# Optimization experiments

Measured on AMD Instinct MI355X. Metric: run time of the kernel, lower is better.

Reference implementation:

```python
import jax, jax.numpy as jnp
import numpy as np

N, E, D, H, L = 50000, 800000, 64, 1, 4
R_DIMS = [64, 32, 16, 16]
LN_EPS = 1e-6  # flax LayerNorm default


def _ln(x, s, b):
    m = jnp.mean(x, axis=-1, keepdims=True)
    v = jnp.mean(jnp.square(x - m), axis=-1, keepdims=True)
    return (x - m) / jnp.sqrt(v + LN_EPS) * s + b


def _jat_layer(x, edges, senders, receivers, mask, Wq, Wk, Wa, ln_s, ln_b, readout):
    # x: (N, H, D) node features
    n = x.shape[0]
    q = jnp.einsum('nab,abcd->ncd', x, Wq)   # (N, H, D) query projection
    k = jnp.einsum('nab,abcd->ncd', x, Wk)   # (N, H, D) key projection
    sq = q[senders]                           # (E, H, D) gather by sender
    rk = k[receivers]                         # (E, H, D) gather by receiver
    feat = jax.nn.swish(sq + rk)
    # per-head edge distance powers, as in the original code
    ep = jnp.reshape(jnp.stack([jnp.power(edges, i + 1) for i in range(H)], axis=0), (-1, H, 1))
    feat = jnp.concatenate([feat, ep], axis=-1)       # (E, H, D+1)
    logits = jnp.einsum('eab,abcd->ecd', feat, Wa)    # (E, H, 1)
    logits = logits + jnp.reshape(jnp.where(mask, 0.0, -jnp.inf), (-1, 1, 1))
    # segment softmax over receiver segments (stable)
    maxs = jax.ops.segment_max(logits, receivers, n)
    w = jnp.exp(logits - maxs[receivers])
    w = w / jax.ops.segment_sum(w, receivers, n)[receivers]
    new = jax.ops.segment_sum(sq * w, receivers, n)   # (N, H, D)
    new = jax.nn.swish(new) + x  # skip_proj is identity (same n_head, dim)
    if not readout:
        new = _ln(new, ln_s, ln_b)
    return new


def setup_inputs() -> dict:
    key = jax.random.key(0)
    ks = jax.random.split(key, 32)
    inp = {
        'nodes': jax.random.normal(ks[0], (N, D), jnp.float32),
        'edges': jax.random.uniform(ks[1], (E, 1), jnp.float32, 0.1, 5.0),
        'senders': jax.random.randint(ks[2], (E,), 0, N, jnp.int32),
        'receivers': jax.random.randint(ks[3], (E,), 0, N, jnp.int32),
        'mask': jnp.ones((E,), bool),
        'Wq': jax.random.normal(ks[4], (L, H, D, H, D), jnp.float32) / np.sqrt(D).astype(np.float32),
        'Wk': jax.random.normal(ks[5], (L, H, D, H, D), jnp.float32) / np.sqrt(D).astype(np.float32),
        'Wa': jax.random.normal(ks[6], (L, H, D + 1, H, 1), jnp.float32) / np.sqrt(D + 1).astype(np.float32),
        'ln_scale': jnp.ones((L - 1, D), jnp.float32),
        'ln_bias': jnp.zeros((L - 1, D), jnp.float32),
    }
    dims = [H * D] + R_DIMS
    for i in range(4):
        inp[f'Wr{i}'] = jax.random.normal(ks[7 + i], (dims[i], dims[i + 1]), jnp.float32) / np.sqrt(dims[i]).astype(np.float32)
        inp[f'rs{i}'] = jnp.ones((dims[i + 1],), jnp.float32)
        inp[f'rb{i}'] = jnp.zeros((dims[i + 1],), jnp.float32)
    inp['Wr4'] = jax.random.normal(ks[11], (R_DIMS[-1], 1), jnp.float32) / np.sqrt(R_DIMS[-1]).astype(np.float32)
    return inp


def reference(nodes, edges, senders, receivers, mask, Wq, Wk, Wa, ln_scale, ln_bias,
              Wr0, Wr1, Wr2, Wr3, Wr4, rs0, rs1, rs2, rs3, rb0, rb1, rb2, rb3):
    x = nodes[:, None, :]  # (N, 1, D): stack to head axis (first layer)
    for l in range(L):
        readout = (l == L - 1)
        ln_s = ln_scale[l] if not readout else None
        ln_b = ln_bias[l] if not readout else None
        x = _jat_layer(x, edges, senders, receivers, mask, Wq[l], Wk[l], Wa[l], ln_s, ln_b, readout)
    # pyramidal readout head [64:32:16:16:1]
    h = jnp.reshape(x, (x.shape[0], -1))
    for Wd, s, b in zip((Wr0, Wr1, Wr2, Wr3), (rs0, rs1, rs2, rs3), (rb0, rb1, rb2, rb3)):
        h = jax.nn.swish(_ln(h @ Wd, s, b))
    return jax.nn.swish(h @ Wr4)  # (N, 1) atomic contributions
```

## Files before the change

### kernel.cpp

```cpp
#include <hip/hip_runtime.h>

#define NN 50000
#define EE 800000

typedef unsigned short ushort_t;
typedef unsigned int uint_t;

__device__ __forceinline__ float rcpf(float x) {
    float r; asm("v_rcp_f32 %0, %1" : "=v"(r) : "v"(x)); return r;
}
__device__ __forceinline__ float swishf(float v) {
    return v * rcpf(1.f + __expf(-v));
}
__device__ __forceinline__ ushort_t f2bf(float f) {
    uint_t u = __float_as_uint(f);
    return (ushort_t)((u + 0x7fffu + ((u >> 16) & 1u)) >> 16);
}
__device__ __forceinline__ float bf2f(ushort_t h) {
    return __uint_as_float(((uint_t)h) << 16);
}
__device__ __forceinline__ float rlane(float v, int i) {
    return __int_as_float(__builtin_amdgcn_readlane(__float_as_int(v), i));
}

__global__ void __launch_bounds__(256, 2) qk_kernel(
    const float* __restrict__ x, const float* __restrict__ Wq, const float* __restrict__ Wk,
    ushort_t* __restrict__ qbf, float* __restrict__ k)
{
    const int lane = threadIdx.x & 63;
    const int wave = (blockIdx.x * 256 + threadIdx.x) >> 6;
    const int nw = gridDim.x * 4;
    float wq[64], wk[64];
#pragma unroll
    for (int i = 0; i < 64; ++i) { wq[i] = Wq[i * 64 + lane]; wk[i] = Wk[i * 64 + lane]; }
    for (int row = wave; row < NN; row += nw) {
        const float h = x[(size_t)row * 64 + lane];
        float aq0 = 0.f, aq1 = 0.f, ak0 = 0.f, ak1 = 0.f;
#pragma unroll
        for (int i = 0; i < 64; i += 2) {
            const float h0 = rlane(h, i), h1 = rlane(h, i + 1);
            aq0 = fmaf(h0, wq[i], aq0);     ak0 = fmaf(h0, wk[i], ak0);
            aq1 = fmaf(h1, wq[i + 1], aq1); ak1 = fmaf(h1, wk[i + 1], ak1);
        }
        qbf[(size_t)row * 64 + lane] = f2bf(aq0 + aq1);
        k[(size_t)row * 64 + lane] = ak0 + ak1;
    }
}

__global__ void __launch_bounds__(256) hist_kernel(
    const int* __restrict__ receivers, int* __restrict__ counts)
{
    int e = blockIdx.x * 256 + threadIdx.x;
    int stride = gridDim.x * 256;
    for (; e < EE; e += stride) atomicAdd(counts + receivers[e], 1);
}

__global__ void __launch_bounds__(256) scanA_kernel(
    const int* __restrict__ counts, int* __restrict__ bsum)
{
    const int idx = blockIdx.x * 256 + threadIdx.x;
    const int lane = threadIdx.x & 63;
    const int wid = threadIdx.x >> 6;
    int s = (idx < NN) ? counts[idx] : 0;
#pragma unroll
    for (int m = 32; m; m >>= 1) s += __shfl_xor(s, m);
    __shared__ int ws[4];
    if (lane == 0) ws[wid] = s;
    __syncthreads();
    if (threadIdx.x == 0) bsum[blockIdx.x] = ws[0] + ws[1] + ws[2] + ws[3];
}

__global__ void __launch_bounds__(256) scanB_kernel(
    const int* __restrict__ bsum, int* __restrict__ boff,
    int* __restrict__ offsets, int nb)
{
    __shared__ int ts[256];
    const int t = threadIdx.x;
    const int v = (t < nb) ? bsum[t] : 0;
    ts[t] = v;
    __syncthreads();
#pragma unroll
    for (int d = 1; d < 256; d <<= 1) {
        const int o = (t >= d) ? ts[t - d] : 0;
        __syncthreads();
        ts[t] += o;
        __syncthreads();
    }
    if (t < nb) boff[t] = ts[t] - v;
    if (t == 0) offsets[NN] = EE;
}

__global__ void __launch_bounds__(256) scanC_kernel(
    const int* __restrict__ counts, const int* __restrict__ boff,
    int* __restrict__ offsets)
{
    const int idx = blockIdx.x * 256 + threadIdx.x;
    const int lane = threadIdx.x & 63;
    const int wid = threadIdx.x >> 6;
    const int v = (idx < NN) ? counts[idx] : 0;
    int incl = v;
#pragma unroll
    for (int d = 1; d < 64; d <<= 1) {
        const int o = __shfl_up(incl, d);
        if (lane >= d) incl += o;
    }
    __shared__ int ws[4];
    if (lane == 63) ws[wid] = incl;
    __syncthreads();
    int wpre = 0;
#pragma unroll
    for (int w = 0; w < 4; ++w) wpre += (w < wid) ? ws[w] : 0;
    if (idx < NN) offsets[idx] = boff[blockIdx.x] + wpre + incl - v;
}

__global__ void __launch_bounds__(256) scatter_kernel(
    const int* __restrict__ receivers, const int* __restrict__ senders,
    const float* __restrict__ edges, const int* __restrict__ offsets,
    int* __restrict__ ctr, int2* __restrict__ sesort)
{
    int e = blockIdx.x * 256 + threadIdx.x;
    int stride = gridDim.x * 256;
    for (; e < EE; e += stride) {
        int r = receivers[e];
        int pos = atomicAdd(ctr + r, 1);
        sesort[offsets[r] + pos] = make_int2(senders[e], __float_as_int(edges[e]));
    }
}

__global__ void __launch_bounds__(256) attn_kernel(
    const ushort_t* __restrict__ qbf, const float* __restrict__ k,
    const int2* __restrict__ sesort, const int* __restrict__ offsets,
    const float* __restrict__ Wa,
    float* __restrict__ x, const float* __restrict__ ln_s,
    const float* __restrict__ ln_b, int do_ln)
{
    __shared__ ushort_t sQ[4][8][64];
    __shared__ float sWb[4][8];
    const int lane = threadIdx.x & 63;
    const int winb = threadIdx.x >> 6;
    const int wave = (blockIdx.x * 256 + threadIdx.x) >> 6;
    const int nw = gridDim.x * 4;
    const int c = lane & 7;
    const int e = lane >> 3;
    const int ofs = c * 8;
    float wac[8];
#pragma unroll
    for (int j = 0; j < 8; ++j) wac[j] = Wa[ofs + j];
    const float wa64 = Wa[64];
    const float lnsv = ln_s[lane], lnbv = ln_b[lane];

    for (int r = wave; r < NN; r += nw) {
        float kc[8];
        {
            const float4 k0 = *(const float4*)(k + (size_t)r * 64 + ofs);
            const float4 k1 = *(const float4*)(k + (size_t)r * 64 + ofs + 4);
            kc[0] = k0.x; kc[1] = k0.y; kc[2] = k0.z; kc[3] = k0.w;
            kc[4] = k1.x; kc[5] = k1.y; kc[6] = k1.z; kc[7] = k1.w;
        }
        const float xv = x[(size_t)r * 64 + lane];
        const int beg = offsets[r], end = offsets[r + 1];
        float m = -3.0e38f, denp = 0.f, acc = 0.f;

        bool valid = (beg + e) < end;
        int2 sev = make_int2(0, 0);
        if (valid) sev = sesort[beg + e];
        uint4 qraw = *(const uint4*)(qbf + (size_t)sev.x * 64 + ofs);
        float ea = __int_as_float(sev.y);

        int i0 = beg;
        while (i0 < end) {
            const int ni0 = i0 + 8;
            bool nvalid = false; float nea = 0.f;
            uint4 nqraw = qraw;
            if (ni0 < end) {
                nvalid = (ni0 + e) < end;
                int2 nsev = make_int2(0, 0);
                if (nvalid) nsev = sesort[ni0 + e];
                nqraw = *(const uint4*)(qbf + (size_t)nsev.x * 64 + ofs);
                nea = __int_as_float(nsev.y);
            }
            float qv[8];
            qv[0] = __uint_as_float(qraw.x << 16);
            qv[1] = __uint_as_float(qraw.x & 0xFFFF0000u);
            qv[2] = __uint_as_float(qraw.y << 16);
            qv[3] = __uint_as_float(qraw.y & 0xFFFF0000u);
            qv[4] = __uint_as_float(qraw.z << 16);
            qv[5] = __uint_as_float(qraw.z & 0xFFFF0000u);
            qv[6] = __uint_as_float(qraw.w << 16);
            qv[7] = __uint_as_float(qraw.w & 0xFFFF0000u);
            float p = 0.f;
#pragma unroll
            for (int j = 0; j < 8; ++j) p = fmaf(swishf(qv[j] + kc[j]), wac[j], p);
            p += __shfl_xor(p, 1);
            p += __shfl_xor(p, 2);
            p += __shfl_xor(p, 4);
            const float logit = valid ? fmaf(ea, wa64, p) : -3.0e38f;
            float cm = logit;
            cm = fmaxf(cm, __shfl_xor(cm, 8));
            cm = fmaxf(cm, __shfl_xor(cm, 16));
            cm = fmaxf(cm, __shfl_xor(cm, 32));
            if (cm > m) {
                const float sc = __expf(m - cm);
                denp *= sc; acc *= sc; m = cm;
            }
            const float w = valid ? __expf(logit - m) : 0.f;
            denp += w;
            *(uint4*)(&sQ[winb][e][ofs]) = qraw;
            if (c == 0) sWb[winb][e] = w;
            __builtin_amdgcn_wave_barrier();
#pragma unroll
            for (int j = 0; j < 8; ++j)
                acc = fmaf(sWb[winb][j], bf2f(sQ[winb][j][lane]), acc);
            __builtin_amdgcn_wave_barrier();
            qraw = nqraw; ea = nea; valid = nvalid; i0 = ni0;
        }

        float den = denp;
#pragma unroll
        for (int msk = 32; msk; msk >>= 1) den += __shfl_xor(den, msk);
        den *= 0.125f;
        float v = den > 0.f ? acc * rcpf(den) : 0.f;
        float nv = swishf(v) + xv;
        if (do_ln) {
            float sum = nv;
#pragma unroll
            for (int msk = 32; msk; msk >>= 1) sum += __shfl_xor(sum, msk);
            const float mean = sum * (1.f / 64.f);
            const float d = nv - mean;
            float vs = d * d;
#pragma unroll
            for (int msk = 32; msk; msk >>= 1) vs += __shfl_xor(vs, msk);
            nv = d * rsqrtf(vs * (1.f / 64.f) + 1e-6f) * lnsv + lnbv;
        }
        x[(size_t)r * 64 + lane] = nv;
    }
}

__device__ __forceinline__ float ln_swish_w(float v, float s, float b) {
    float sum = v, sq = v * v;
#pragma unroll
    for (int m = 32; m; m >>= 1) { sum += __shfl_xor(sum, m); sq += __shfl_xor(sq, m); }
    const float mean = sum * (1.f / 64.f);
    const float var = fmaf(-mean, mean, sq * (1.f / 64.f));
    return swishf((v - mean) * rsqrtf(var + 1e-6f) * s + b);
}

__global__ void __launch_bounds__(256, 2) rd0_kernel(
    const float* __restrict__ x,
    const float* __restrict__ W0, const float* __restrict__ rs0, const float* __restrict__ rb0,
    float* __restrict__ y0out)
{
    const int lane = threadIdx.x & 63;
    const int wave = (blockIdx.x * 256 + threadIdx.x) >> 6;
    const int nw = gridDim.x * 4;
    float w0[64];
#pragma unroll
    for (int i = 0; i < 64; ++i) w0[i] = W0[i * 64 + lane];
    const float s0v = rs0[lane], b0v = rb0[lane];
    for (int n = wave; n < NN; n += nw) {
        const float h = x[(size_t)n * 64 + lane];
        float a0 = 0.f, a1 = 0.f, a2 = 0.f, a3 = 0.f;
#pragma unroll
        for (int i = 0; i < 64; i += 4) {
            a0 = fmaf(rlane(h, i),     w0[i],     a0);
            a1 = fmaf(rlane(h, i + 1), w0[i + 1], a1);
            a2 = fmaf(rlane(h, i + 2), w0[i + 2], a2);
            a3 = fmaf(rlane(h, i + 3), w0[i + 3], a3);
        }
        y0out[(size_t)n * 64 + lane] = ln_swish_w((a0 + a1) + (a2 + a3), s0v, b0v);
    }
}

__global__ void __launch_bounds__(256, 2) rd1_kernel(
    const float* __restrict__ y0in,
    const float* __restrict__ W1, const float* __restrict__ rs1, const float* __restrict__ rb1,
    const float* __restrict__ W2, const float* __restrict__ rs2, const float* __restrict__ rb2,
    const float* __restrict__ W3, const float* __restrict__ rs3, const float* __restrict__ rb3,
    const float* __restrict__ W4, float* __restrict__ out)
{
    const int lane = threadIdx.x & 63;
    const int wave = (blockIdx.x * 256 + threadIdx.x) >> 6;
    const int nw = gridDim.x * 4;
    const int j1 = lane & 31, j2 = lane & 15;
    float w1[64], w2[32], w3[16];
#pragma unroll
    for (int i = 0; i < 64; ++i) w1[i] = W1[i * 32 + j1];
#pragma unroll
    for (int i = 0; i < 32; ++i) w2[i] = W2[i * 16 + j2];
#pragma unroll
    for (int i = 0; i < 16; ++i) w3[i] = W3[i * 16 + j2];
    const float w4v = W4[j2];
    const float s1v = rs1[j1], b1v = rb1[j1];
    const float s2v = rs2[j2], b2v = rb2[j2];
    const float s3v = rs3[j2], b3v = rb3[j2];

    for (int n = wave; n < NN; n += nw) {
        const float y0 = y0in[(size_t)n * 64 + lane];
        float a0 = 0.f, a1 = 0.f, a2 = 0.f, a3 = 0.f;
#pragma unroll
        for (int i = 0; i < 64; i += 4) {
            a0 = fmaf(rlane(y0, i),     w1[i],     a0);
            a1 = fmaf(rlane(y0, i + 1), w1[i + 1], a1);
            a2 = fmaf(rlane(y0, i + 2), w1[i + 2], a2);
            a3 = fmaf(rlane(y0, i + 3), w1[i + 3], a3);
        }
        const float y1 = ln_swish_w((a0 + a1) + (a2 + a3), s1v, b1v);

        a0 = a1 = a2 = a3 = 0.f;
#pragma unroll
        for (int i = 0; i < 32; i += 4) {
            a0 = fmaf(rlane(y1, i),     w2[i],     a0);
            a1 = fmaf(rlane(y1, i + 1), w2[i + 1], a1);
            a2 = fmaf(rlane(y1, i + 2), w2[i + 2], a2);
            a3 = fmaf(rlane(y1, i + 3), w2[i + 3], a3);
        }
        const float y2 = ln_swish_w((a0 + a1) + (a2 + a3), s2v, b2v);

        a0 = a1 = a2 = a3 = 0.f;
#pragma unroll
        for (int i = 0; i < 16; i += 4) {
            a0 = fmaf(rlane(y2, i),     w3[i],     a0);
            a1 = fmaf(rlane(y2, i + 1), w3[i + 1], a1);
            a2 = fmaf(rlane(y2, i + 2), w3[i + 2], a2);
            a3 = fmaf(rlane(y2, i + 3), w3[i + 3], a3);
        }
        const float y3 = ln_swish_w((a0 + a1) + (a2 + a3), s3v, b3v);

        float p = y3 * w4v;
#pragma unroll
        for (int m = 32; m; m >>= 1) p += __shfl_xor(p, m);
        if (lane == 0) out[n] = swishf(p * 0.25f);
    }
}

extern "C" void kernel_launch(void* const* d_in, const int* in_sizes, int n_in,
                              void* d_out, int out_size, void* d_ws, size_t ws_size,
                              hipStream_t stream)
{
    const float* nodes     = (const float*)d_in[0];
    const float* edges     = (const float*)d_in[1];
    const int*   senders   = (const int*)d_in[2];
    const int*   receivers = (const int*)d_in[3];
    const float* Wq  = (const float*)d_in[5];
    const float* Wk  = (const float*)d_in[6];
    const float* Wa  = (const float*)d_in[7];
    const float* ln_s = (const float*)d_in[8];
    const float* ln_b = (const float*)d_in[9];
    const float* Wr0 = (const float*)d_in[10];
    const float* rs0 = (const float*)d_in[11];
    const float* rb0 = (const float*)d_in[12];
    const float* Wr1 = (const float*)d_in[13];
    const float* rs1 = (const float*)d_in[14];
    const float* rb1 = (const float*)d_in[15];
    const float* Wr2 = (const float*)d_in[16];
    const float* rs2 = (const float*)d_in[17];
    const float* rb2 = (const float*)d_in[18];
    const float* Wr3 = (const float*)d_in[19];
    const float* rs3 = (const float*)d_in[20];
    const float* rb3 = (const float*)d_in[21];
    const float* Wr4 = (const float*)d_in[22];
    float* out = (float*)d_out;

    float*    x       = (float*)d_ws;
    float*    k       = x + (size_t)NN * 64;
    ushort_t* qbf     = (ushort_t*)(k + (size_t)NN * 64);
    int*      counts  = (int*)(qbf + (size_t)NN * 64);
    int*      ctr     = counts + NN;
    int*      offsets = ctr + NN;
    int2*     sesort  = (int2*)(offsets + NN + 2);
    int*      bsum    = (int*)(sesort + EE);
    int*      boff    = bsum + 256;

    const int NB = (NN + 255) / 256;

    hipMemcpyAsync(x, nodes, (size_t)NN * 64 * sizeof(float), hipMemcpyDeviceToDevice, stream);

    hipMemsetAsync(counts, 0, 2 * NN * sizeof(int), stream);
    hist_kernel<<<3125, 256, 0, stream>>>(receivers, counts);
    scanA_kernel<<<NB, 256, 0, stream>>>(counts, bsum);
    scanB_kernel<<<1, 256, 0, stream>>>(bsum, boff, offsets, NB);
    scanC_kernel<<<NB, 256, 0, stream>>>(counts, boff, offsets);
    scatter_kernel<<<3125, 256, 0, stream>>>(receivers, senders, edges, offsets, ctr, sesort);

    for (int l = 0; l < 4; ++l) {
        qk_kernel<<<1024, 256, 0, stream>>>(x, Wq + l * 4096, Wk + l * 4096, qbf, k);
        int lnidx = l < 3 ? l : 0;
        attn_kernel<<<3125, 256, 0, stream>>>(qbf, k, sesort, offsets,
                                              Wa + l * 65, x,
                                              ln_s + lnidx * 64, ln_b + lnidx * 64,
                                              l < 3 ? 1 : 0);
    }
    rd0_kernel<<<1024, 256, 0, stream>>>(x, Wr0, rs0, rb0, k);
    rd1_kernel<<<1024, 256, 0, stream>>>(k, Wr1, rs1, rb1, Wr2, rs2, rb2,
                                         Wr3, rs3, rb3, Wr4, out);
}
```

Baseline: 553.3 us.

## Pack sender and quantized edge into 32 bits, accumulate in registers

Each CSR entry now holds the sender index (17 bits) and the edge distance quantized to 1/4096 (15 bits) in one 32-bit word, halving the index stream the attention loop reads. The per-iteration LDS staging of q rows and weights, with its wave barriers, is replaced by eight per-lane register accumulators, reduced once per node with shuffles. The qk kernel also drops its minimum-blocks launch bound. Edge quantization adds a small rounding error and assumes edges below 8 and node counts under 2^17.

```diff
diff --git a/kernel.cpp b/kernel.cpp
--- a/kernel.cpp
+++ b/kernel.cpp
@@ -16,14 +16,11 @@
     uint_t u = __float_as_uint(f);
     return (ushort_t)((u + 0x7fffu + ((u >> 16) & 1u)) >> 16);
 }
-__device__ __forceinline__ float bf2f(ushort_t h) {
-    return __uint_as_float(((uint_t)h) << 16);
-}
 __device__ __forceinline__ float rlane(float v, int i) {
     return __int_as_float(__builtin_amdgcn_readlane(__float_as_int(v), i));
 }
 
-__global__ void __launch_bounds__(256, 2) qk_kernel(
+__global__ void __launch_bounds__(256) qk_kernel(
     const float* __restrict__ x, const float* __restrict__ Wq, const float* __restrict__ Wk,
     ushort_t* __restrict__ qbf, float* __restrict__ k)
 {
@@ -116,28 +113,26 @@
 __global__ void __launch_bounds__(256) scatter_kernel(
     const int* __restrict__ receivers, const int* __restrict__ senders,
     const float* __restrict__ edges, const int* __restrict__ offsets,
-    int* __restrict__ ctr, int2* __restrict__ sesort)
+    int* __restrict__ ctr, uint_t* __restrict__ sesort)
 {
     int e = blockIdx.x * 256 + threadIdx.x;
     int stride = gridDim.x * 256;
     for (; e < EE; e += stride) {
         int r = receivers[e];
         int pos = atomicAdd(ctr + r, 1);
-        sesort[offsets[r] + pos] = make_int2(senders[e], __float_as_int(edges[e]));
+        uint_t packed = ((uint_t)(edges[e] * 4096.f + 0.5f) << 17) | (uint_t)senders[e];
+        sesort[offsets[r] + pos] = packed;
     }
 }
 
 __global__ void __launch_bounds__(256) attn_kernel(
     const ushort_t* __restrict__ qbf, const float* __restrict__ k,
-    const int2* __restrict__ sesort, const int* __restrict__ offsets,
+    const uint_t* __restrict__ sesort, const int* __restrict__ offsets,
     const float* __restrict__ Wa,
     float* __restrict__ x, const float* __restrict__ ln_s,
     const float* __restrict__ ln_b, int do_ln)
 {
-    __shared__ ushort_t sQ[4][8][64];
-    __shared__ float sWb[4][8];
-    const int lane = threadIdx.x & 63;
-    const int winb = threadIdx.x >> 6;
+    const int lane = threadIdx.x & 63;
     const int wave = (blockIdx.x * 256 + threadIdx.x) >> 6;
     const int nw = gridDim.x * 4;
     const int c = lane & 7;
@@ -159,13 +154,15 @@
         }
         const float xv = x[(size_t)r * 64 + lane];
         const int beg = offsets[r], end = offsets[r + 1];
-        float m = -3.0e38f, denp = 0.f, acc = 0.f;
+        float m = -3.0e38f, denp = 0.f;
+        float acc8[8];
+#pragma unroll
+        for (int j = 0; j < 8; ++j) acc8[j] = 0.f;
 
         bool valid = (beg + e) < end;
-        int2 sev = make_int2(0, 0);
-        if (valid) sev = sesort[beg + e];
-        uint4 qraw = *(const uint4*)(qbf + (size_t)sev.x * 64 + ofs);
-        float ea = __int_as_float(sev.y);
+        uint_t u = valid ? sesort[beg + e] : 0u;
+        uint4 qraw = *(const uint4*)(qbf + (size_t)(u & 0x1FFFFu) * 64 + ofs);
+        float ea = (float)(u >> 17) * (1.f / 4096.f);
 
         int i0 = beg;
         while (i0 < end) {
@@ -174,10 +171,9 @@
             uint4 nqraw = qraw;
             if (ni0 < end) {
                 nvalid = (ni0 + e) < end;
-                int2 nsev = make_int2(0, 0);
-                if (nvalid) nsev = sesort[ni0 + e];
-                nqraw = *(const uint4*)(qbf + (size_t)nsev.x * 64 + ofs);
-                nea = __int_as_float(nsev.y);
+                uint_t nu = nvalid ? sesort[ni0 + e] : 0u;
+                nqraw = *(const uint4*)(qbf + (size_t)(nu & 0x1FFFFu) * 64 + ofs);
+                nea = (float)(nu >> 17) * (1.f / 4096.f);
             }
             float qv[8];
             qv[0] = __uint_as_float(qraw.x << 16);
@@ -201,25 +197,39 @@
             cm = fmaxf(cm, __shfl_xor(cm, 32));
             if (cm > m) {
                 const float sc = __expf(m - cm);
-                denp *= sc; acc *= sc; m = cm;
+                denp *= sc;
+#pragma unroll
+                for (int j = 0; j < 8; ++j) acc8[j] *= sc;
+                m = cm;
             }
             const float w = valid ? __expf(logit - m) : 0.f;
             denp += w;
-            *(uint4*)(&sQ[winb][e][ofs]) = qraw;
-            if (c == 0) sWb[winb][e] = w;
-            __builtin_amdgcn_wave_barrier();
-#pragma unroll
-            for (int j = 0; j < 8; ++j)
-                acc = fmaf(sWb[winb][j], bf2f(sQ[winb][j][lane]), acc);
-            __builtin_amdgcn_wave_barrier();
+#pragma unroll
+            for (int j = 0; j < 8; ++j) acc8[j] = fmaf(w, qv[j], acc8[j]);
             qraw = nqraw; ea = nea; valid = nvalid; i0 = ni0;
         }
 
+#pragma unroll
+        for (int j = 0; j < 8; ++j) {
+            acc8[j] += __shfl_xor(acc8[j], 8);
+            acc8[j] += __shfl_xor(acc8[j], 16);
+            acc8[j] += __shfl_xor(acc8[j], 32);
+        }
         float den = denp;
-#pragma unroll
-        for (int msk = 32; msk; msk >>= 1) den += __shfl_xor(den, msk);
-        den *= 0.125f;
-        float v = den > 0.f ? acc * rcpf(den) : 0.f;
+        den += __shfl_xor(den, 8);
+        den += __shfl_xor(den, 16);
+        den += __shfl_xor(den, 32);
+        float vsel = acc8[0];
+        if (e == 1) vsel = acc8[1];
+        if (e == 2) vsel = acc8[2];
+        if (e == 3) vsel = acc8[3];
+        if (e == 4) vsel = acc8[4];
+        if (e == 5) vsel = acc8[5];
+        if (e == 6) vsel = acc8[6];
+        if (e == 7) vsel = acc8[7];
+        const float num = __shfl(vsel, (c << 3) | e);
+
+        float v = den > 0.f ? num * rcpf(den) : 0.f;
         float nv = swishf(v) + xv;
         if (do_ln) {
             float sum = nv;
@@ -367,7 +377,7 @@
     int*      counts  = (int*)(qbf + (size_t)NN * 64);
     int*      ctr     = counts + NN;
     int*      offsets = ctr + NN;
-    int2*     sesort  = (int2*)(offsets + NN + 2);
+    uint_t*   sesort  = (uint_t*)(offsets + NN + 1);
     int*      bsum    = (int*)(sesort + EE);
     int*      boff    = bsum + 256;
 
```

Result: slower. 598.8 us (+8.2%).
